# Kernel optimization log

Measured on AMD Instinct MI355X. Metric: run time of the kernel, lower is better.

Reference implementation:

```python
import jax, jax.numpy as jnp
import numpy as np

N_NODES = 50000
N_EDGES = 800000
D = 96
H2 = 32
OUT = 4


def _glorot(key, shape):
    fan_in, fan_out = shape[0], shape[1]
    lim = (6.0 / (fan_in + fan_out)) ** 0.5
    return jax.random.uniform(key, shape, jnp.float32, -lim, lim)


def setup_inputs() -> dict:
    key = jax.random.key(0)
    ks = jax.random.split(key, 12)
    x = jax.random.normal(ks[0], (N_NODES, D), jnp.float32)
    edge_index = jax.random.randint(ks[1], (2, N_EDGES), 0, N_NODES, jnp.int32)
    return {
        "x": x,
        "edge_index": edge_index,
        "eps1": jnp.float32(0.0),
        "eps2": jnp.float32(0.0),
        "W1a": _glorot(ks[2], (D, D)),  "b1a": jnp.zeros((D,), jnp.float32),
        "W1b": _glorot(ks[3], (D, D)),  "b1b": jnp.zeros((D,), jnp.float32),
        "W2a": _glorot(ks[4], (D, H2)), "b2a": jnp.zeros((H2,), jnp.float32),
        "W2b": _glorot(ks[5], (H2, H2)),"b2b": jnp.zeros((H2,), jnp.float32),
        "Wh": _glorot(ks[6], (H2, OUT)),"bh": jnp.zeros((OUT,), jnp.float32),
    }


def _gin_agg(h, src, dst):
    # sum_{j in N(i)} h_j : gather source features, scatter-add to destination
    return jax.ops.segment_sum(h[src], dst, num_segments=N_NODES)


def reference(x, edge_index, eps1, eps2, W1a, b1a, W1b, b1b, W2a, b2a, W2b, b2b, Wh, bh):
    src, dst = edge_index[0], edge_index[1]

    # GIN layer 1: mlp1((1+eps1)*x + agg(x)), then outer ReLU (dropout is eval-mode identity)
    z = (1.0 + eps1) * x + _gin_agg(x, src, dst)           # [N, D]
    h = jax.nn.relu(z @ W1a + b1a) @ W1b + b1b             # mlp1
    h = jax.nn.relu(h)

    # GIN layer 2: mlp2((1+eps2)*h + agg(h)), then outer ReLU
    z2 = (1.0 + eps2) * h + _gin_agg(h, src, dst)          # [N, D]
    h2 = jax.nn.relu(z2 @ W2a + b2a) @ W2b + b2b           # mlp2 -> [N, 32]
    h2 = jax.nn.relu(h2)

    return h2 @ Wh + bh                                    # [N, 4]
```

## Files before the change

### kernel.cpp

```cpp
#include <hip/hip_runtime.h>

#define NN 50000
#define NE 800000
#define DD 96
#define HH 32
#define OO 4
#define ELLW 64
#define NBUCK 196
#define BCAP 8192

typedef unsigned short ushort_t;
typedef unsigned int uint_t;
typedef __attribute__((ext_vector_type(8))) short short8;
typedef __attribute__((ext_vector_type(4))) float f32x4;

__device__ inline ushort_t f2bf(float f) {
    uint_t b = __float_as_uint(f);
    return (ushort_t)((b + 0x7fffu + ((b >> 16) & 1u)) >> 16);
}

__device__ inline void addbf8(float* a, uint4 u) {
    a[0] += __uint_as_float(u.x << 16);
    a[1] += __uint_as_float(u.x & 0xffff0000u);
    a[2] += __uint_as_float(u.y << 16);
    a[3] += __uint_as_float(u.y & 0xffff0000u);
    a[4] += __uint_as_float(u.z << 16);
    a[5] += __uint_as_float(u.z & 0xffff0000u);
    a[6] += __uint_as_float(u.w << 16);
    a[7] += __uint_as_float(u.w & 0xffff0000u);
}


#define BA_B   196
#define WF_B   6

__global__ void k_pre(const int* __restrict__ edges, int* __restrict__ bcnt,
                      uint_t* __restrict__ packed,
                      const float* __restrict__ W1b, const float* __restrict__ W2a,
                      ushort_t* __restrict__ wf) {
    int b = blockIdx.x;
    if (b < BA_B) {
        __shared__ int hist[NBUCK];
        __shared__ int basesh[NBUCK];
        int thr = threadIdx.x;
        if (thr < NBUCK) hist[thr] = 0;
        __syncthreads();
#pragma unroll
        for (int k = 0; k < 4; ++k) {
            int t4 = b * 1024 + k * 256 + thr;
            if (t4 < NE / 4) {
                int4 tt = ((const int4*)(edges + NE))[t4];
                atomicAdd(&hist[tt.x >> 8], 1);
                atomicAdd(&hist[tt.y >> 8], 1);
                atomicAdd(&hist[tt.z >> 8], 1);
                atomicAdd(&hist[tt.w >> 8], 1);
            }
        }
        __syncthreads();
        if (thr < NBUCK) {
            int c = hist[thr];
            basesh[thr] = c ? atomicAdd(&bcnt[thr], c) : 0;
        }
        __syncthreads();
        if (thr < NBUCK) hist[thr] = 0;
        __syncthreads();
#pragma unroll
        for (int k = 0; k < 4; ++k) {
            int t4 = b * 1024 + k * 256 + thr;
            if (t4 < NE / 4) {
                int4 ss = ((const int4*)edges)[t4];
                int4 tt = ((const int4*)(edges + NE))[t4];
                int b0 = tt.x >> 8, b1 = tt.y >> 8, b2 = tt.z >> 8, b3 = tt.w >> 8;
                int p0 = basesh[b0] + atomicAdd(&hist[b0], 1);
                int p1 = basesh[b1] + atomicAdd(&hist[b1], 1);
                int p2 = basesh[b2] + atomicAdd(&hist[b2], 1);
                int p3 = basesh[b3] + atomicAdd(&hist[b3], 1);
                if (p0 < BCAP) packed[(size_t)b0 * BCAP + p0] = ((uint_t)ss.x << 8) | (tt.x & 255);
                if (p1 < BCAP) packed[(size_t)b1 * BCAP + p1] = ((uint_t)ss.y << 8) | (tt.y & 255);
                if (p2 < BCAP) packed[(size_t)b2 * BCAP + p2] = ((uint_t)ss.z << 8) | (tt.z & 255);
                if (p3 < BCAP) packed[(size_t)b3 * BCAP + p3] = ((uint_t)ss.w << 8) | (tt.w & 255);
            }
        }
        return;
    }
    b -= BA_B;
    int tw = b * 256 + threadIdx.x;
    if (tw < 1152 + 384) {
        const float* Wsrc; ushort_t* dst; int KOUT, fl;
        if (tw < 1152) { Wsrc = W1b; dst = wf;        KOUT = DD; fl = tw; }
        else           { Wsrc = W2a; dst = wf + 9216; KOUT = HH; fl = tw - 1152; }
        int lane = fl & 63;
        int fc = fl >> 6;
        int c = fc % 3, nt = fc / 3;
        int kb = c * 32 + (lane >> 4) * 8;
        int col = nt * 16 + (lane & 15);
        ushort_t v[8];
#pragma unroll
        for (int j = 0; j < 8; ++j)
            v[j] = f2bf(Wsrc[(size_t)(kb + j) * KOUT + col]);
        *(uint4*)(dst + (size_t)fl * 8) = *(uint4*)v;
    }
}


#define MT1    (NN / 16)
#define MFMA1_B ((MT1 + 3) / 4)

__global__ void k_main(const int* __restrict__ bcnt, const uint_t* __restrict__ packed,
                       ushort_t* __restrict__ ell, int* __restrict__ deg,
                       const float* __restrict__ x, const float* __restrict__ W1a,
                       ushort_t* __restrict__ y1) {
    __shared__ __align__(16) ushort_t lds[1152 * 8];
    int b = blockIdx.x;
    int thr = threadIdx.x;
    if (b < NBUCK) {
        int* curL = (int*)lds;
        int n0 = b * 256;
        curL[thr] = 0;
        __syncthreads();
        int cnt = min(bcnt[b], BCAP);
        const uint_t* pk = packed + (size_t)b * BCAP;
        for (int e = thr; e < cnt; e += 256) {
            uint_t u = pk[e];
            int doff = u & 255;
            int src = u >> 8;
            int p = atomicAdd(&curL[doff], 1);
            if (p < ELLW) ell[(size_t)(n0 + doff) * ELLW + p] = (ushort_t)src;
        }
        __syncthreads();
        if (n0 + thr < NN) deg[n0 + thr] = curL[thr];
        return;
    }
    b -= NBUCK;
    constexpr int KC = 3, NT = 6;
    for (int fl = thr; fl < 1152; fl += 256) {
        int lane_f = fl & 63;
        int fc = fl >> 6;
        int c = fc % 3, nt = fc / 3;
        int kb = c * 32 + (lane_f >> 4) * 8;
        int col = nt * 16 + (lane_f & 15);
        ushort_t v[8];
#pragma unroll
        for (int j = 0; j < 8; ++j)
            v[j] = f2bf(W1a[(size_t)(kb + j) * DD + col]);
        *(uint4*)(lds + (size_t)fl * 8) = *(uint4*)v;
    }
    __syncthreads();

    int lane = thr & 63;
    int widx = thr >> 6;
    int tile = b * 4 + widx;
    if (tile >= MT1) return;
    int row0 = tile * 16;
    int q = lane >> 4;
    int l16 = lane & 15;

    short8 bf[NT][KC];
#pragma unroll
    for (int nt = 0; nt < NT; ++nt)
#pragma unroll
        for (int c = 0; c < KC; ++c)
            bf[nt][c] = *(short8*)(lds + ((size_t)(nt * 3 + c) * 64 + lane) * 8);

    short8 af[KC];
#pragma unroll
    for (int c = 0; c < KC; ++c) {
        const float* ap = x + (size_t)(row0 + l16) * DD + c * 32 + q * 8;
        float4 f0 = *(const float4*)ap;
        float4 f1 = *(const float4*)(ap + 4);
        ushort_t v[8] = {f2bf(f0.x), f2bf(f0.y), f2bf(f0.z), f2bf(f0.w),
                         f2bf(f1.x), f2bf(f1.y), f2bf(f1.z), f2bf(f1.w)};
        af[c] = *(short8*)v;
    }

    f32x4 acc[NT];
#pragma unroll
    for (int nt = 0; nt < NT; ++nt) acc[nt] = (f32x4){0.f, 0.f, 0.f, 0.f};
#pragma unroll
    for (int nt = 0; nt < NT; ++nt)
#pragma unroll
        for (int c = 0; c < KC; ++c)
            acc[nt] = __builtin_amdgcn_mfma_f32_16x16x32_bf16(af[c], bf[nt][c], acc[nt], 0, 0, 0);

#pragma unroll
    for (int nt = 0; nt < NT; ++nt) {
        int s = nt >> 1;
        int c32 = (nt & 1) * 16 + l16;
#pragma unroll
        for (int r = 0; r < 4; ++r)
            y1[(size_t)s * NN * 32 + (size_t)(row0 + q * 4 + r) * 32 + c32] = f2bf(acc[nt][r]);
    }
}


#define HSTRIDE 104

__global__ void k_aggmm(const ushort_t* __restrict__ y1, const int* __restrict__ deg,
                        const ushort_t* __restrict__ ell, const float* __restrict__ eps_p,
                        const float* __restrict__ b1a, const ushort_t* __restrict__ wf,
                        const float* __restrict__ b1b, ushort_t* __restrict__ y2) {
    constexpr int KC = 3, NT1 = 6, NT2 = 2;
    __shared__ __align__(16) ushort_t hT[64 * HSTRIDE];
    int thr = threadIdx.x;
    int g = thr >> 2;
    int u = thr & 3;
    int i = blockIdx.x * 64 + g;

    if (i < NN) {
        const ushort_t* er = ell + (size_t)i * ELLW;
        int d = min(deg[i], ELLW);
        float e = 1.0f + eps_p[0];
        const float4* b4 = (const float4*)b1a;
        ushort_t* dstg = &hT[g * HSTRIDE + u * 8];
#pragma unroll 1
        for (int s = 0; s < 3; ++s) {
            const uint4* ysS = (const uint4*)(y1 + (size_t)s * NN * 32);
            float a0[8] = {0,0,0,0,0,0,0,0}, a1[8] = {0,0,0,0,0,0,0,0};
            float a2[8] = {0,0,0,0,0,0,0,0}, a3[8] = {0,0,0,0,0,0,0,0};
            int p = 0;
            for (; p + 3 < d; p += 4) {
                int s0 = er[p], s1 = er[p + 1], s2 = er[p + 2], s3 = er[p + 3];
                uint4 f0 = ysS[(size_t)s0 * 4 + u];
                uint4 f1 = ysS[(size_t)s1 * 4 + u];
                uint4 f2 = ysS[(size_t)s2 * 4 + u];
                uint4 f3 = ysS[(size_t)s3 * 4 + u];
                addbf8(a0, f0); addbf8(a1, f1); addbf8(a2, f2); addbf8(a3, f3);
            }
            for (; p < d; ++p) addbf8(a0, ysS[(size_t)er[p] * 4 + u]);

            uint4 su = ysS[(size_t)i * 4 + u];
            float s8[8];
            s8[0] = __uint_as_float(su.x << 16); s8[1] = __uint_as_float(su.x & 0xffff0000u);
            s8[2] = __uint_as_float(su.y << 16); s8[3] = __uint_as_float(su.y & 0xffff0000u);
            s8[4] = __uint_as_float(su.z << 16); s8[5] = __uint_as_float(su.z & 0xffff0000u);
            s8[6] = __uint_as_float(su.w << 16); s8[7] = __uint_as_float(su.w & 0xffff0000u);
            float4 bl = b4[s * 8 + u * 2];
            float4 bh2 = b4[s * 8 + u * 2 + 1];
            float bb[8] = {bl.x, bl.y, bl.z, bl.w, bh2.x, bh2.y, bh2.z, bh2.w};
            ushort_t r[8];
#pragma unroll
            for (int k = 0; k < 8; ++k) {
                float vv = fmaf(e, s8[k], (a0[k] + a1[k]) + (a2[k] + a3[k])) + bb[k];
                r[k] = f2bf(fmaxf(vv, 0.0f));
            }
            *(uint4*)(dstg + s * 32) = *(uint4*)r;
        }
    }
    __syncthreads();

    int lane = thr & 63;
    int widx = thr >> 6;
    int tile = blockIdx.x * 4 + widx;
    if (tile >= MT1) return;
    int row0 = tile * 16;
    int q = lane >> 4;
    int l16 = lane & 15;
    const short8* bfp1 = (const short8*)wf;
    const short8* bfp2 = (const short8*)(wf + 9216);

    short8 bf[NT1][KC];
#pragma unroll
    for (int nt = 0; nt < NT1; ++nt)
#pragma unroll
        for (int c = 0; c < KC; ++c)
            bf[nt][c] = bfp1[(nt * KC + c) * 64 + lane];

    short8 af2[KC];
#pragma unroll
    for (int c = 0; c < KC; ++c) {
        uint4 av = *(const uint4*)&hT[(widx * 16 + l16) * HSTRIDE + c * 32 + q * 8];
        af2[c] = *(short8*)&av;
    }

    f32x4 acc[NT1];
#pragma unroll
    for (int nt = 0; nt < NT1; ++nt) acc[nt] = (f32x4){0.f, 0.f, 0.f, 0.f};
#pragma unroll
    for (int nt = 0; nt < NT1; ++nt)
#pragma unroll
        for (int c = 0; c < KC; ++c)
            acc[nt] = __builtin_amdgcn_mfma_f32_16x16x32_bf16(af2[c], bf[nt][c], acc[nt], 0, 0, 0);

    __syncthreads();
#pragma unroll
    for (int nt = 0; nt < NT1; ++nt) {
        int col = nt * 16 + l16;
        float bv = b1b[col];
#pragma unroll
        for (int r = 0; r < 4; ++r)
            hT[(widx * 16 + q * 4 + r) * HSTRIDE + col] = f2bf(fmaxf(acc[nt][r] + bv, 0.0f));
    }
    __syncthreads();

    short8 af3[KC];
#pragma unroll
    for (int c = 0; c < KC; ++c) {
        uint4 av = *(const uint4*)&hT[(widx * 16 + l16) * HSTRIDE + c * 32 + q * 8];
        af3[c] = *(short8*)&av;
    }
    short8 bf2[NT2][KC];
#pragma unroll
    for (int nt = 0; nt < NT2; ++nt)
#pragma unroll
        for (int c = 0; c < KC; ++c)
            bf2[nt][c] = bfp2[(nt * KC + c) * 64 + lane];

    f32x4 acc2[NT2];
#pragma unroll
    for (int nt = 0; nt < NT2; ++nt) acc2[nt] = (f32x4){0.f, 0.f, 0.f, 0.f};
#pragma unroll
    for (int nt = 0; nt < NT2; ++nt)
#pragma unroll
        for (int c = 0; c < KC; ++c)
            acc2[nt] = __builtin_amdgcn_mfma_f32_16x16x32_bf16(af3[c], bf2[nt][c], acc2[nt], 0, 0, 0);

#pragma unroll
    for (int nt = 0; nt < NT2; ++nt) {
        int col = nt * 16 + l16;
#pragma unroll
        for (int r = 0; r < 4; ++r)
            y2[(size_t)(row0 + q * 4 + r) * HH + col] = f2bf(acc2[nt][r]);
    }
}


#define TSTRIDE 36
#define ATR 16

__global__ void k_aggtail(const ushort_t* __restrict__ y2, const int* __restrict__ deg,
                          const ushort_t* __restrict__ ell, const float* __restrict__ eps_p,
                          const float* __restrict__ b2a, const float* __restrict__ W2b,
                          const float* __restrict__ b2b, const float* __restrict__ Wh,
                          const float* __restrict__ bhp, float* __restrict__ out) {
    __shared__ float t2f[ATR * TSTRIDE];
    int row = threadIdx.x >> 4;
    int sub = threadIdx.x & 15;
    int jg = sub & 3;
    int part = sub >> 2;
    int i = blockIdx.x * ATR + row;
    bool live = i < NN;

    if (live) {
        const uint4* y4 = (const uint4*)y2;
        const ushort_t* er = ell + (size_t)i * ELLW;
        int d = min(deg[i], ELLW);
        float a0[8] = {0,0,0,0,0,0,0,0}, a1[8] = {0,0,0,0,0,0,0,0};
        int p = part;
        for (; p + 4 < d; p += 8) {
            int s0 = er[p], s1 = er[p + 4];
            uint4 f0 = y4[(size_t)s0 * 4 + jg];
            uint4 f1 = y4[(size_t)s1 * 4 + jg];
            addbf8(a0, f0); addbf8(a1, f1);
        }
        for (; p < d; p += 4) addbf8(a0, y4[(size_t)er[p] * 4 + jg]);

        float s[8];
#pragma unroll
        for (int k = 0; k < 8; ++k) {
            s[k] = a0[k] + a1[k];
            s[k] += __shfl_xor(s[k], 4);
            s[k] += __shfl_xor(s[k], 8);
        }
        if (part == 0) {
            uint4 su = y4[(size_t)i * 4 + jg];
            float s8[8];
            s8[0] = __uint_as_float(su.x << 16); s8[1] = __uint_as_float(su.x & 0xffff0000u);
            s8[2] = __uint_as_float(su.y << 16); s8[3] = __uint_as_float(su.y & 0xffff0000u);
            s8[4] = __uint_as_float(su.z << 16); s8[5] = __uint_as_float(su.z & 0xffff0000u);
            s8[6] = __uint_as_float(su.w << 16); s8[7] = __uint_as_float(su.w & 0xffff0000u);
            float4 bl = ((const float4*)b2a)[2 * jg];
            float4 bhv = ((const float4*)b2a)[2 * jg + 1];
            float bb[8] = {bl.x, bl.y, bl.z, bl.w, bhv.x, bhv.y, bhv.z, bhv.w};
            float e = 1.0f + eps_p[0];
#pragma unroll
            for (int k = 0; k < 8; ++k) {
                float vv = fmaf(e, s8[k], s[k]) + bb[k];
                t2f[row * TSTRIDE + jg * 8 + k] = fmaxf(vv, 0.0f);
            }
        }
    }
    __syncthreads();

    float o[OO] = {0.f, 0.f, 0.f, 0.f};
    if (live) {
        const float* tr = &t2f[row * TSTRIDE];
#pragma unroll
        for (int jj = 0; jj < 2; ++jj) {
            int j = sub * 2 + jj;
            float acc = b2b[j];
#pragma unroll 8
            for (int k = 0; k < HH; ++k)
                acc = fmaf(tr[k], W2b[k * HH + j], acc);
            acc = fmaxf(acc, 0.0f);
#pragma unroll
            for (int oo = 0; oo < OO; ++oo)
                o[oo] = fmaf(acc, Wh[j * OO + oo], o[oo]);
        }
    }
#pragma unroll
    for (int oo = 0; oo < OO; ++oo) {
        o[oo] += __shfl_xor(o[oo], 1);
        o[oo] += __shfl_xor(o[oo], 2);
        o[oo] += __shfl_xor(o[oo], 4);
        o[oo] += __shfl_xor(o[oo], 8);
    }
    if (live && sub == 0) {
        float4 ov = {o[0] + bhp[0], o[1] + bhp[1], o[2] + bhp[2], o[3] + bhp[3]};
        ((float4*)out)[i] = ov;
    }
}


extern "C" void kernel_launch(void* const* d_in, const int* in_sizes, int n_in,
                              void* d_out, int out_size, void* d_ws, size_t ws_size,
                              hipStream_t stream) {
    const float* x    = (const float*)d_in[0];
    const int*   edges= (const int*)d_in[1];
    const float* eps1 = (const float*)d_in[2];
    const float* eps2 = (const float*)d_in[3];
    const float* W1a  = (const float*)d_in[4];
    const float* b1a  = (const float*)d_in[5];
    const float* W1b  = (const float*)d_in[6];
    const float* b1b  = (const float*)d_in[7];
    const float* W2a  = (const float*)d_in[8];
    const float* b2a  = (const float*)d_in[9];
    const float* W2b  = (const float*)d_in[10];
    const float* b2b  = (const float*)d_in[11];
    const float* Wh   = (const float*)d_in[12];
    const float* bh   = (const float*)d_in[13];

    auto al = [](size_t n) { return (n + 255) / 256 * 256; };
    char* w = (char*)d_ws;
    int*      bcnt   = (int*)w;      w += al((size_t)NBUCK * 4);
    uint_t*   packed = (uint_t*)w;   w += al((size_t)NBUCK * BCAP * 4);
    int*      deg    = (int*)w;      w += al((size_t)NN * 4);
    ushort_t* ell    = (ushort_t*)w; w += al((size_t)NN * ELLW * 2);
    ushort_t* wf     = (ushort_t*)w; w += al((size_t)(9216 + 3072) * 2);
    ushort_t* y1     = (ushort_t*)w; w += al((size_t)NN * DD * 2);
    ushort_t* y2     = (ushort_t*)w; w += al((size_t)NN * HH * 2);

    const int B = 256;

    hipMemsetAsync(bcnt, 0, (size_t)NBUCK * 4, stream);
    k_pre<<<BA_B + WF_B, B, 0, stream>>>(edges, bcnt, packed, W1b, W2a, wf);
    k_main<<<NBUCK + MFMA1_B, B, 0, stream>>>(bcnt, packed, ell, deg, x, W1a, y1);
    k_aggmm<<<MFMA1_B, B, 0, stream>>>(y1, deg, ell, eps1, b1a, wf, b1b, y2);
    k_aggtail<<<(NN + ATR - 1) / ATR, B, 0, stream>>>(y2, deg, ell, eps2, b2a, W2b, b2b,
                                                      Wh, bh, (float*)d_out);
}
```

Measured before the change: 184.5 us.

## Replace scalar tail MLP with bf16 MFMA and stage ELL rows in LDS

```diff
diff --git a/kernel.cpp b/kernel.cpp
--- a/kernel.cpp
+++ b/kernel.cpp
@@ -32,11 +32,12 @@
 
 
 #define BA_B   196
-#define WF_B   6
+#define WF_B   7
 
 __global__ void k_pre(const int* __restrict__ edges, int* __restrict__ bcnt,
                       uint_t* __restrict__ packed,
                       const float* __restrict__ W1b, const float* __restrict__ W2a,
+                      const float* __restrict__ W2b, const float* __restrict__ Wh,
                       ushort_t* __restrict__ wf) {
     int b = blockIdx.x;
     if (b < BA_B) {
@@ -85,20 +86,46 @@
     }
     b -= BA_B;
     int tw = b * 256 + threadIdx.x;
-    if (tw < 1152 + 384) {
-        const float* Wsrc; ushort_t* dst; int KOUT, fl;
-        if (tw < 1152) { Wsrc = W1b; dst = wf;        KOUT = DD; fl = tw; }
-        else           { Wsrc = W2a; dst = wf + 9216; KOUT = HH; fl = tw - 1152; }
-        int lane = fl & 63;
-        int fc = fl >> 6;
-        int c = fc % 3, nt = fc / 3;
-        int kb = c * 32 + (lane >> 4) * 8;
-        int col = nt * 16 + (lane & 15);
+    if (tw < 1728) {
         ushort_t v[8];
-#pragma unroll
-        for (int j = 0; j < 8; ++j)
-            v[j] = f2bf(Wsrc[(size_t)(kb + j) * KOUT + col]);
-        *(uint4*)(dst + (size_t)fl * 8) = *(uint4*)v;
+        ushort_t* dst;
+        if (tw < 1152) {
+            int fl = tw;
+            int lane = fl & 63, fc = fl >> 6;
+            int c = fc % 3, nt = fc / 3;
+            int kb = c * 32 + (lane >> 4) * 8;
+            int col = nt * 16 + (lane & 15);
+#pragma unroll
+            for (int j = 0; j < 8; ++j) v[j] = f2bf(W1b[(size_t)(kb + j) * DD + col]);
+            dst = wf + (size_t)fl * 8;
+        } else if (tw < 1536) {
+            int fl = tw - 1152;
+            int lane = fl & 63, fc = fl >> 6;
+            int c = fc % 3, nt = fc / 3;
+            int kb = c * 32 + (lane >> 4) * 8;
+            int col = nt * 16 + (lane & 15);
+#pragma unroll
+            for (int j = 0; j < 8; ++j) v[j] = f2bf(W2a[(size_t)(kb + j) * HH + col]);
+            dst = wf + 9216 + (size_t)fl * 8;
+        } else if (tw < 1664) {
+            int fl = tw - 1536;
+            int lane = fl & 63, nt = fl >> 6;
+            int kb = (lane >> 4) * 8;
+            int col = nt * 16 + (lane & 15);
+#pragma unroll
+            for (int j = 0; j < 8; ++j) v[j] = f2bf(W2b[(size_t)(kb + j) * HH + col]);
+            dst = wf + 12288 + (size_t)fl * 8;
+        } else {
+            int fl = tw - 1664;
+            int lane = fl;
+            int kb = (lane >> 4) * 8;
+            int col = lane & 15;
+#pragma unroll
+            for (int j = 0; j < 8; ++j)
+                v[j] = (col < OO) ? f2bf(Wh[(size_t)(kb + j) * OO + col]) : (ushort_t)0;
+            dst = wf + 13312 + (size_t)fl * 8;
+        }
+        *(uint4*)dst = *(uint4*)v;
     }
 }
 
@@ -201,14 +228,29 @@
                         const float* __restrict__ b1b, ushort_t* __restrict__ y2) {
     constexpr int KC = 3, NT1 = 6, NT2 = 2;
     __shared__ __align__(16) ushort_t hT[64 * HSTRIDE];
+    __shared__ __align__(16) ushort_t erL[64 * ELLW];
+    __shared__ int degL[64];
     int thr = threadIdx.x;
+    int i0 = blockIdx.x * 64;
+
+    for (int t = thr; t < 64 * 8; t += 256) {
+        int r = t >> 3, c8 = t & 7;
+        int ii = i0 + r;
+        uint4 val;
+        if (ii < NN) val = ((const uint4*)(ell + (size_t)ii * ELLW))[c8];
+        else { val.x = 0; val.y = 0; val.z = 0; val.w = 0; }
+        *(uint4*)&erL[r * 64 + c8 * 8] = val;
+    }
+    if (thr < 64) degL[thr] = (i0 + thr < NN) ? min(deg[i0 + thr], ELLW) : 0;
+    __syncthreads();
+
     int g = thr >> 2;
     int u = thr & 3;
-    int i = blockIdx.x * 64 + g;
+    int i = i0 + g;
 
     if (i < NN) {
-        const ushort_t* er = ell + (size_t)i * ELLW;
-        int d = min(deg[i], ELLW);
+        const ushort_t* er = &erL[g * 64];
+        int d = degL[g];
         float e = 1.0f + eps_p[0];
         const float4* b4 = (const float4*)b1a;
         ushort_t* dstg = &hT[g * HSTRIDE + u * 8];
@@ -324,89 +366,112 @@
 }
 
 
-#define TSTRIDE 36
-#define ATR 16
-
-__global__ void k_aggtail(const ushort_t* __restrict__ y2, const int* __restrict__ deg,
-                          const ushort_t* __restrict__ ell, const float* __restrict__ eps_p,
-                          const float* __restrict__ b2a, const float* __restrict__ W2b,
-                          const float* __restrict__ b2b, const float* __restrict__ Wh,
-                          const float* __restrict__ bhp, float* __restrict__ out) {
-    __shared__ float t2f[ATR * TSTRIDE];
-    int row = threadIdx.x >> 4;
-    int sub = threadIdx.x & 15;
-    int jg = sub & 3;
-    int part = sub >> 2;
-    int i = blockIdx.x * ATR + row;
-    bool live = i < NN;
-
-    if (live) {
+#define TS2 40
+
+__global__ void k_agg2tail(const ushort_t* __restrict__ y2, const int* __restrict__ deg,
+                           const ushort_t* __restrict__ ell, const float* __restrict__ eps_p,
+                           const float* __restrict__ b2a, const float* __restrict__ b2b,
+                           const float* __restrict__ bhp, const ushort_t* __restrict__ wf,
+                           float* __restrict__ out) {
+    __shared__ __align__(16) ushort_t erL[64 * ELLW];
+    __shared__ int degL[64];
+    __shared__ __align__(16) ushort_t t2T[64 * TS2];
+    __shared__ __align__(16) ushort_t hB[4][16 * TS2];
+    int thr = threadIdx.x;
+    int i0 = blockIdx.x * 64;
+
+    for (int t = thr; t < 64 * 8; t += 256) {
+        int r = t >> 3, c8 = t & 7;
+        int ii = i0 + r;
+        uint4 val;
+        if (ii < NN) val = ((const uint4*)(ell + (size_t)ii * ELLW))[c8];
+        else { val.x = 0; val.y = 0; val.z = 0; val.w = 0; }
+        *(uint4*)&erL[r * 64 + c8 * 8] = val;
+    }
+    if (thr < 64) degL[thr] = (i0 + thr < NN) ? min(deg[i0 + thr], ELLW) : 0;
+    __syncthreads();
+
+    int g = thr >> 2;
+    int u = thr & 3;
+    int i = i0 + g;
+
+    if (i < NN) {
+        const ushort_t* er = &erL[g * 64];
+        int d = degL[g];
         const uint4* y4 = (const uint4*)y2;
-        const ushort_t* er = ell + (size_t)i * ELLW;
-        int d = min(deg[i], ELLW);
         float a0[8] = {0,0,0,0,0,0,0,0}, a1[8] = {0,0,0,0,0,0,0,0};
-        int p = part;
-        for (; p + 4 < d; p += 8) {
-            int s0 = er[p], s1 = er[p + 4];
-            uint4 f0 = y4[(size_t)s0 * 4 + jg];
-            uint4 f1 = y4[(size_t)s1 * 4 + jg];
-            addbf8(a0, f0); addbf8(a1, f1);
-        }
-        for (; p < d; p += 4) addbf8(a0, y4[(size_t)er[p] * 4 + jg]);
-
-        float s[8];
+        float a2[8] = {0,0,0,0,0,0,0,0}, a3[8] = {0,0,0,0,0,0,0,0};
+        int p = 0;
+        for (; p + 3 < d; p += 4) {
+            int s0 = er[p], s1 = er[p + 1], s2 = er[p + 2], s3 = er[p + 3];
+            uint4 f0 = y4[(size_t)s0 * 4 + u];
+            uint4 f1 = y4[(size_t)s1 * 4 + u];
+            uint4 f2 = y4[(size_t)s2 * 4 + u];
+            uint4 f3 = y4[(size_t)s3 * 4 + u];
+            addbf8(a0, f0); addbf8(a1, f1); addbf8(a2, f2); addbf8(a3, f3);
+        }
+        for (; p < d; ++p) addbf8(a0, y4[(size_t)er[p] * 4 + u]);
+
+        uint4 su = y4[(size_t)i * 4 + u];
+        float s8[8];
+        s8[0] = __uint_as_float(su.x << 16); s8[1] = __uint_as_float(su.x & 0xffff0000u);
+        s8[2] = __uint_as_float(su.y << 16); s8[3] = __uint_as_float(su.y & 0xffff0000u);
+        s8[4] = __uint_as_float(su.z << 16); s8[5] = __uint_as_float(su.z & 0xffff0000u);
+        s8[6] = __uint_as_float(su.w << 16); s8[7] = __uint_as_float(su.w & 0xffff0000u);
+        float4 bl = ((const float4*)b2a)[u * 2];
+        float4 bh2 = ((const float4*)b2a)[u * 2 + 1];
+        float bb[8] = {bl.x, bl.y, bl.z, bl.w, bh2.x, bh2.y, bh2.z, bh2.w};
+        float e = 1.0f + eps_p[0];
+        ushort_t r[8];
 #pragma unroll
         for (int k = 0; k < 8; ++k) {
-            s[k] = a0[k] + a1[k];
-            s[k] += __shfl_xor(s[k], 4);
-            s[k] += __shfl_xor(s[k], 8);
-        }
-        if (part == 0) {
-            uint4 su = y4[(size_t)i * 4 + jg];
-            float s8[8];
-            s8[0] = __uint_as_float(su.x << 16); s8[1] = __uint_as_float(su.x & 0xffff0000u);
-            s8[2] = __uint_as_float(su.y << 16); s8[3] = __uint_as_float(su.y & 0xffff0000u);
-            s8[4] = __uint_as_float(su.z << 16); s8[5] = __uint_as_float(su.z & 0xffff0000u);
-            s8[6] = __uint_as_float(su.w << 16); s8[7] = __uint_as_float(su.w & 0xffff0000u);
-            float4 bl = ((const float4*)b2a)[2 * jg];
-            float4 bhv = ((const float4*)b2a)[2 * jg + 1];
-            float bb[8] = {bl.x, bl.y, bl.z, bl.w, bhv.x, bhv.y, bhv.z, bhv.w};
-            float e = 1.0f + eps_p[0];
-#pragma unroll
-            for (int k = 0; k < 8; ++k) {
-                float vv = fmaf(e, s8[k], s[k]) + bb[k];
-                t2f[row * TSTRIDE + jg * 8 + k] = fmaxf(vv, 0.0f);
-            }
-        }
-    }
-    __syncthreads();
-
-    float o[OO] = {0.f, 0.f, 0.f, 0.f};
-    if (live) {
-        const float* tr = &t2f[row * TSTRIDE];
-#pragma unroll
-        for (int jj = 0; jj < 2; ++jj) {
-            int j = sub * 2 + jj;
-            float acc = b2b[j];
-#pragma unroll 8
-            for (int k = 0; k < HH; ++k)
-                acc = fmaf(tr[k], W2b[k * HH + j], acc);
-            acc = fmaxf(acc, 0.0f);
-#pragma unroll
-            for (int oo = 0; oo < OO; ++oo)
-                o[oo] = fmaf(acc, Wh[j * OO + oo], o[oo]);
-        }
-    }
-#pragma unroll
-    for (int oo = 0; oo < OO; ++oo) {
-        o[oo] += __shfl_xor(o[oo], 1);
-        o[oo] += __shfl_xor(o[oo], 2);
-        o[oo] += __shfl_xor(o[oo], 4);
-        o[oo] += __shfl_xor(o[oo], 8);
-    }
-    if (live && sub == 0) {
-        float4 ov = {o[0] + bhp[0], o[1] + bhp[1], o[2] + bhp[2], o[3] + bhp[3]};
-        ((float4*)out)[i] = ov;
+            float vv = fmaf(e, s8[k], (a0[k] + a1[k]) + (a2[k] + a3[k])) + bb[k];
+            r[k] = f2bf(fmaxf(vv, 0.0f));
+        }
+        *(uint4*)&t2T[g * TS2 + u * 8] = *(uint4*)r;
+    }
+    __syncthreads();
+
+    int lane = thr & 63;
+    int widx = thr >> 6;
+    int tile = blockIdx.x * 4 + widx;
+    if (tile >= MT1) return;
+    int row0 = tile * 16;
+    int q = lane >> 4;
+    int l16 = lane & 15;
+
+    uint4 av = *(const uint4*)&t2T[(widx * 16 + l16) * TS2 + q * 8];
+    short8 afA = *(short8*)&av;
+    const short8* bfW2b = (const short8*)(wf + 12288);
+    const short8* bfWh  = (const short8*)(wf + 13312);
+
+    f32x4 acc2[2];
+#pragma unroll
+    for (int nt = 0; nt < 2; ++nt) {
+        acc2[nt] = (f32x4){0.f, 0.f, 0.f, 0.f};
+        acc2[nt] = __builtin_amdgcn_mfma_f32_16x16x32_bf16(afA, bfW2b[nt * 64 + lane],
+                                                           acc2[nt], 0, 0, 0);
+    }
+
+#pragma unroll
+    for (int nt = 0; nt < 2; ++nt) {
+        int col = nt * 16 + l16;
+        float bv = b2b[col];
+#pragma unroll
+        for (int r = 0; r < 4; ++r)
+            hB[widx][(q * 4 + r) * TS2 + col] = f2bf(fmaxf(acc2[nt][r] + bv, 0.0f));
+    }
+
+    uint4 av2 = *(const uint4*)&hB[widx][l16 * TS2 + q * 8];
+    short8 afH = *(short8*)&av2;
+    f32x4 acch = (f32x4){0.f, 0.f, 0.f, 0.f};
+    acch = __builtin_amdgcn_mfma_f32_16x16x32_bf16(afH, bfWh[lane], acch, 0, 0, 0);
+
+    if (l16 < OO) {
+        float bv = bhp[l16];
+#pragma unroll
+        for (int r = 0; r < 4; ++r)
+            out[(size_t)(row0 + q * 4 + r) * OO + l16] = acch[r] + bv;
     }
 }
 
@@ -435,16 +500,16 @@
     uint_t*   packed = (uint_t*)w;   w += al((size_t)NBUCK * BCAP * 4);
     int*      deg    = (int*)w;      w += al((size_t)NN * 4);
     ushort_t* ell    = (ushort_t*)w; w += al((size_t)NN * ELLW * 2);
-    ushort_t* wf     = (ushort_t*)w; w += al((size_t)(9216 + 3072) * 2);
+    ushort_t* wf     = (ushort_t*)w; w += al((size_t)13824 * 2);
     ushort_t* y1     = (ushort_t*)w; w += al((size_t)NN * DD * 2);
     ushort_t* y2     = (ushort_t*)w; w += al((size_t)NN * HH * 2);
 
     const int B = 256;
 
     hipMemsetAsync(bcnt, 0, (size_t)NBUCK * 4, stream);
-    k_pre<<<BA_B + WF_B, B, 0, stream>>>(edges, bcnt, packed, W1b, W2a, wf);
+    k_pre<<<BA_B + WF_B, B, 0, stream>>>(edges, bcnt, packed, W1b, W2a, W2b, Wh, wf);
     k_main<<<NBUCK + MFMA1_B, B, 0, stream>>>(bcnt, packed, ell, deg, x, W1a, y1);
     k_aggmm<<<MFMA1_B, B, 0, stream>>>(y1, deg, ell, eps1, b1a, wf, b1b, y2);
-    k_aggtail<<<(NN + ATR - 1) / ATR, B, 0, stream>>>(y2, deg, ell, eps2, b2a, W2b, b2b,
-                                                      Wh, bh, (float*)d_out);
-}
+    k_agg2tail<<<(NN + 63) / 64, B, 0, stream>>>(y2, deg, ell, eps2, b2a, b2b, bh, wf,
+                                                 (float*)d_out);
+}
```

Result: faster. 153.3 us (-16.9%).
